# Kernel optimization log

Hardware: AMD Instinct MI355X
Metric: run time of the kernel (lower is better)

## Reference

```python
import jax, jax.numpy as jnp
import numpy as np

# OPT-1.3b-like attention dims
B, S, E, NH, HD = 1, 2048, 2048, 32, 64
Q_BITS, R_BITS, BASE_GS, R_GS = 1, 3, 16, 16


def quotrem_fake_quantize(x, q_bits=Q_BITS, r_bits=R_BITS, base_gs=BASE_GS, r_gs=R_GS):
    r_max = 2 ** (r_bits - 1) - 1
    r_min = -r_max - 1
    eps = 1e-8
    shape = x.shape
    H = shape[-1]
    xg = x.reshape(shape[:-1] + (H // base_gs, base_gs))  # [..., G_base, base_gs]
    max_abs = jnp.maximum(jnp.max(jnp.abs(xg), axis=-1, keepdims=True), eps)
    if q_bits == 1:
        log2_max = jnp.log2(max_abs)
        base_floor = jnp.exp2(jnp.floor(log2_max))
        base_ceil = jnp.exp2(jnp.ceil(log2_max))
        base = jnp.where(jnp.abs(max_abs - base_floor) <= jnp.abs(base_ceil - max_abs),
                         base_floor, base_ceil)
        base = jnp.clip(base, 1.0, 128.0)
        max_pos = jnp.max(xg, axis=-1, keepdims=True)
        min_val = jnp.min(xg, axis=-1, keepdims=True)
        sign_flag = jnp.where(jnp.abs(max_pos) >= jnp.abs(min_val), 1.0, -1.0)
        q = (xg * sign_flag >= base / 2.0).astype(x.dtype)
        q_scaled = q * sign_flag * base
    else:
        q_max = 2 ** (q_bits - 1) - 1
        threshold = max_abs / q_max
        base = jnp.full_like(threshold, 64.0)
        for b in (32.0, 16.0, 8.0, 4.0, 2.0):
            base = jnp.where(threshold <= b, jnp.full_like(threshold, b), base)
        q = jnp.clip(jnp.round(xg / base), -q_max, q_max)
        q_scaled = q * base
    r = (xg - q_scaled).reshape(shape)
    rg = r.reshape(shape[:-1] + (H // r_gs, r_gs))  # [..., G_r, r_gs]
    max_abs_r = jnp.maximum(jnp.max(jnp.abs(rg), axis=-1, keepdims=True), eps)
    scale_r = max_abs_r / r_max
    r_q = jnp.clip(jnp.round(rg / scale_r), r_min, r_max)
    r_dq = (r_q * scale_r).reshape(shape)
    return q_scaled.reshape(shape) + r_dq


def setup_inputs() -> dict:
    key = jax.random.key(0)
    ks = jax.random.split(key, 9)
    w = lambda k: jax.random.normal(k, (E, E), dtype=jnp.float32) * 0.02
    b = lambda k: jax.random.normal(k, (E,), dtype=jnp.float32) * 0.02
    return {
        "hidden_states": jax.random.normal(ks[0], (B, S, E), dtype=jnp.float32),
        "Wq": w(ks[1]), "bq": b(ks[2]),
        "Wk": w(ks[3]), "bk": b(ks[4]),
        "Wv": w(ks[5]), "bv": b(ks[6]),
        "Wo": w(ks[7]), "bo": b(ks[8]),
    }


def reference(hidden_states, Wq, bq, Wk, bk, Wv, bv, Wo, bo):
    scaling = HD ** -0.5
    heads = lambda x: x.reshape(B, S, NH, HD).transpose(0, 2, 1, 3)  # [B,NH,S,HD]
    q = heads((hidden_states @ Wq.T + bq) * scaling)
    k = quotrem_fake_quantize(heads(hidden_states @ Wk.T + bk))
    v = quotrem_fake_quantize(heads(hidden_states @ Wv.T + bv))
    scores = jnp.einsum('bhqd,bhkd->bhqk', q, k)
    idx = jnp.arange(S)
    scores = jnp.where(idx[:, None] >= idx[None, :], scores, -jnp.inf)  # causal
    attn = jax.nn.softmax(scores, axis=-1)
    out = jnp.einsum('bhqk,bhkd->bhqd', attn, v).transpose(0, 2, 1, 3).reshape(B, S, E)
    return out @ Wo.T + bo
```

## Files before the change

### kernel.cpp

```cpp
#include <hip/hip_runtime.h>
#include <math.h>

#define SEQ 2048
#define EMB 2048
#define NHEAD 32
#define HDIM 64

typedef unsigned short u16;
typedef _Float16 half8 __attribute__((ext_vector_type(8)));
typedef _Float16 half4 __attribute__((ext_vector_type(4)));
typedef __attribute__((ext_vector_type(4))) float floatx4;

__device__ __forceinline__ floatx4 mfma_f16(half8 a, half8 b, floatx4 c) {
    return __builtin_amdgcn_mfma_f32_16x16x32_f16(a, b, c, 0, 0, 0);
}
__device__ __forceinline__ void load16(const u16* g, u16* l) {
    __builtin_amdgcn_global_load_lds(
        (const __attribute__((address_space(1))) unsigned int*)g,
        (__attribute__((address_space(3))) unsigned int*)l, 16, 0, 0);
}
__device__ __forceinline__ u16 h2u(_Float16 h) { return *reinterpret_cast<u16*>(&h); }

__global__ __launch_bounds__(256)
void cvt4(const float* __restrict__ X0, u16* __restrict__ Y0,
          const float* __restrict__ X1, u16* __restrict__ Y1,
          const float* __restrict__ X2, u16* __restrict__ Y2,
          const float* __restrict__ X3, u16* __restrict__ Y3)
{
    const float* Xs[4] = {X0, X1, X2, X3};
    u16* Ys[4] = {Y0, Y1, Y2, Y3};
    const float* X = Xs[blockIdx.y];
    u16* Y = Ys[blockIdx.y];
    const int i = (blockIdx.x * 256 + threadIdx.x) * 4;
    float4 v = *reinterpret_cast<const float4*>(X + i);
    half4 hv;
    hv.x = (_Float16)v.x; hv.y = (_Float16)v.y;
    hv.z = (_Float16)v.z; hv.w = (_Float16)v.w;
    *reinterpret_cast<half4*>(Y + i) = hv;
}

__global__ __launch_bounds__(256)
void gemm16(const u16* __restrict__ A,
            const u16* __restrict__ B0, const u16* __restrict__ B1,
            const u16* __restrict__ B2,
            const float* __restrict__ bk, const float* __restrict__ bv,
            const float* __restrict__ bq,
            float* __restrict__ F0, float* __restrict__ F1,
            u16* __restrict__ Qb)
{
    __shared__ __align__(16) u16 As[128 * 64];
    __shared__ __align__(16) u16 Bs[128 * 64];

    const int tid = threadIdx.x;
    const int w = tid >> 6, lane = tid & 63;
    const int quad = lane >> 4, colk = lane & 15;
    const int bn = blockIdx.x, bm = blockIdx.y, z = blockIdx.z;
    const int wm = (w & 1) * 64, wn = (w >> 1) * 64;

    const u16* Bg = (z == 0) ? B0 : (z == 1) ? B1 : B2;

    const int srow = tid >> 3, sphy = tid & 7;
    const int sLog = (sphy - srow) & 7;
    size_t agof[4], bgof[4];
    int ldst[4];
    #pragma unroll
    for (int p = 0; p < 4; ++p) {
        const int row = srow + 32 * p;
        agof[p] = (size_t)(bm * 128 + row) * EMB + sLog * 8;
        bgof[p] = (size_t)(bn * 128 + row) * EMB + sLog * 8;
        ldst[p] = (tid + 256 * p) * 8;
    }

    const int aoct0 = ((quad + colk) & 7) * 8;
    const int aoct1 = ((quad + 4 + colk) & 7) * 8;

    floatx4 acc[4][4];
    #pragma unroll
    for (int i = 0; i < 4; ++i)
        #pragma unroll
        for (int j = 0; j < 4; ++j) acc[i][j] = (floatx4){0.f, 0.f, 0.f, 0.f};

    for (int kt = 0; kt < 2048; kt += 64) {
        __syncthreads();
        #pragma unroll
        for (int p = 0; p < 4; ++p) {
            load16(A  + agof[p] + kt, As + ldst[p]);
            load16(Bg + bgof[p] + kt, Bs + ldst[p]);
        }
        __syncthreads();

        half8 a0[4], a1[4], b0[4], b1[4];
        #pragma unroll
        for (int i = 0; i < 4; ++i) {
            a0[i] = *reinterpret_cast<const half8*>(&As[(wm + 16*i + colk) * 64 + aoct0]);
            a1[i] = *reinterpret_cast<const half8*>(&As[(wm + 16*i + colk) * 64 + aoct1]);
        }
        #pragma unroll
        for (int j = 0; j < 4; ++j) {
            b0[j] = *reinterpret_cast<const half8*>(&Bs[(wn + 16*j + colk) * 64 + aoct0]);
            b1[j] = *reinterpret_cast<const half8*>(&Bs[(wn + 16*j + colk) * 64 + aoct1]);
        }
        #pragma unroll
        for (int i = 0; i < 4; ++i)
            #pragma unroll
            for (int j = 0; j < 4; ++j) {
                acc[i][j] = mfma_f16(a0[i], b0[j], acc[i][j]);
                acc[i][j] = mfma_f16(a1[i], b1[j], acc[i][j]);
            }
    }

    const float* bias = (z == 0) ? bk : (z == 1) ? bv : bq;
    #pragma unroll
    for (int i = 0; i < 4; ++i) {
        const int row = bm * 128 + wm + 16*i + 4*quad;
        #pragma unroll
        for (int j = 0; j < 4; ++j) {
            const int col = bn * 128 + wn + 16*j + colk;
            const float bv2 = bias[col];
            #pragma unroll
            for (int r = 0; r < 4; ++r) {
                const size_t idx = (size_t)(row + r) * EMB + col;
                if (z == 2)
                    ((_Float16*)Qb)[idx] = (_Float16)((acc[i][j][r] + bv2) * 0.125f);
                else
                    ((z == 0) ? F0 : F1)[idx] = acc[i][j][r] + bv2;
            }
        }
    }
}

__device__ __forceinline__ void quotrem16(float* x)
{
    float maxabs = 1e-8f, maxpos = -INFINITY, minval = INFINITY;
    #pragma unroll
    for (int i = 0; i < 16; ++i) {
        maxabs = fmaxf(maxabs, fabsf(x[i]));
        maxpos = fmaxf(maxpos, x[i]);
        minval = fminf(minval, x[i]);
    }
    const float lg = log2f(maxabs);
    const float bfl = exp2f(floorf(lg));
    const float bcl = exp2f(ceilf(lg));
    float base = (fabsf(maxabs - bfl) <= fabsf(bcl - maxabs)) ? bfl : bcl;
    base = fminf(fmaxf(base, 1.0f), 128.0f);
    const float sgn = (fabsf(maxpos) >= fabsf(minval)) ? 1.0f : -1.0f;
    const float hb = 0.5f * base, sb = sgn * base;

    float qs[16], r[16], maxr = 1e-8f;
    #pragma unroll
    for (int i = 0; i < 16; ++i) {
        qs[i] = (x[i] * sgn >= hb) ? sb : 0.0f;
        r[i]  = x[i] - qs[i];
        maxr  = fmaxf(maxr, fabsf(r[i]));
    }
    const float scale = maxr / 3.0f;
    #pragma unroll
    for (int i = 0; i < 16; ++i) {
        float rq = rintf(r[i] / scale);
        rq = fminf(fmaxf(rq, -4.0f), 3.0f);
        x[i] = qs[i] + rq * scale;
    }
}

__global__ __launch_bounds__(256)
void quant_kv(const float* __restrict__ FK, u16* __restrict__ Kb,
              const float* __restrict__ FV, u16* __restrict__ Vt,
              const float* __restrict__ Wo, u16* __restrict__ Wo16)
{
    __shared__ u16 T[64 * 264];
    const int bid = blockIdx.x, t = threadIdx.x;

    if (bid >= 1280) {
        const int i = ((bid - 1280) * 256 + t) * 4;
        float4 v = *reinterpret_cast<const float4*>(Wo + i);
        half4 hv;
        hv.x = (_Float16)v.x; hv.y = (_Float16)v.y;
        hv.z = (_Float16)v.z; hv.w = (_Float16)v.w;
        *reinterpret_cast<half4*>(Wo16 + i) = hv;
        return;
    }

    if (bid < 1024) {
        const int g = bid * 256 + t;
        const float* p = FK + (size_t)g * 16;
        float x[16];
        #pragma unroll
        for (int i = 0; i < 16; i += 4)
            *reinterpret_cast<float4*>(&x[i]) = *reinterpret_cast<const float4*>(p + i);
        quotrem16(x);
        _Float16* o = (_Float16*)Kb + (size_t)g * 16;
        #pragma unroll
        for (int i = 0; i < 16; ++i) o[i] = (_Float16)x[i];
        return;
    }

    const int l = bid - 1024;
    const int sb = l >> 5, h = l & 31;
    const float* src = FV + (size_t)(sb * 256 + t) * EMB + h * HDIM;

    #pragma unroll
    for (int g4 = 0; g4 < 4; ++g4) {
        float x[16];
        #pragma unroll
        for (int i = 0; i < 16; i += 4)
            *reinterpret_cast<float4*>(&x[i]) =
                *reinterpret_cast<const float4*>(src + g4 * 16 + i);
        quotrem16(x);
        #pragma unroll
        for (int i = 0; i < 16; ++i)
            T[(g4 * 16 + i) * 264 + t] = h2u((_Float16)x[i]);
    }
    __syncthreads();

    const int d = t >> 2, seg = t & 3;
    u16* dst = Vt + (size_t)(h * HDIM + d) * SEQ + sb * 256 + seg * 64;
    #pragma unroll
    for (int jj = 0; jj < 8; ++jj)
        *reinterpret_cast<half8*>(dst + jj * 8) =
            *reinterpret_cast<const half8*>(&T[d * 264 + seg * 64 + jj * 8]);
}

__global__ __launch_bounds__(256)
void flash128(const u16* __restrict__ Qb, const u16* __restrict__ Kb,
              const u16* __restrict__ Vt, u16* __restrict__ Ob)
{
    __shared__ __align__(16) u16 Ks[128 * 64];
    __shared__ __align__(16) u16 Vs[64 * 128];
    __shared__ __align__(16) u16 Ps[64 * 136];

    const int tid = threadIdx.x;
    const int w = tid >> 6, lane = tid & 63;
    const int quad = lane >> 4, colk = lane & 15;
    const int id = blockIdx.x;
    const int h = (id & 7) * 4 + ((id >> 3) & 3);
    const int pairb = id >> 5;

    int krow[4], koff[4], vd[4], voff[4];
    #pragma unroll
    for (int p = 0; p < 4; ++p) {
        const int c = tid + p * 256;
        krow[p] = c >> 3;
        koff[p] = (((c & 7) - krow[p]) & 7) * 8;
        vd[p]   = c >> 4;
        voff[p] = (((c & 15) - vd[p]) & 15) * 8;
    }
    const int ldb0 = w * 512;
    const int kp0 = ((quad + colk) & 7) * 8;
    const int kp1 = ((quad + 4 + colk) & 7) * 8;

    #pragma unroll
    for (int pass = 0; pass < 2; ++pass) {
        const int qt = pass ? (31 - pairb) : pairb;
        const int nw = (qt + 2) >> 1;
        const int qrow_g = qt * 64 + 16 * w + colk;

        __syncthreads();
        #pragma unroll
        for (int p = 0; p < 2; ++p) {
            const int c = tid + p * 256, row = c >> 3, cq = c & 7;
            *reinterpret_cast<half8*>(&Ps[row * 136 + cq * 8]) =
                *reinterpret_cast<const half8*>(&Qb[(size_t)(qt * 64 + row) * EMB + h * HDIM + cq * 8]);
        }
        __syncthreads();
        const half8 qb0 = *reinterpret_cast<const half8*>(&Ps[(16*w + colk) * 136 + quad * 8]);
        const half8 qb1 = *reinterpret_cast<const half8*>(&Ps[(16*w + colk) * 136 + 32 + quad * 8]);

        floatx4 o[4];
        #pragma unroll
        for (int t = 0; t < 4; ++t) o[t] = (floatx4){0.f, 0.f, 0.f, 0.f};
        float lsum = 0.f;

        for (int kw = 0; kw < nw; ++kw) {
            __syncthreads();
            #pragma unroll
            for (int p = 0; p < 4; ++p) {
                load16(Kb + (size_t)(kw * 128 + krow[p]) * EMB + h * HDIM + koff[p],
                       Ks + p * 2048 + ldb0);
                load16(Vt + (size_t)(h * HDIM + vd[p]) * SEQ + kw * 128 + voff[p],
                       Vs + p * 2048 + ldb0);
            }
            __syncthreads();

            floatx4 s[8];
            #pragma unroll
            for (int t = 0; t < 8; ++t) {
                const half8 kb0 = *reinterpret_cast<const half8*>(&Ks[(16*t + colk) * 64 + kp0]);
                const half8 kb1 = *reinterpret_cast<const half8*>(&Ks[(16*t + colk) * 64 + kp1]);
                floatx4 zz = (floatx4){0.f, 0.f, 0.f, 0.f};
                zz = mfma_f16(kb0, qb0, zz);
                s[t] = mfma_f16(kb1, qb1, zz);
            }
            if (kw == nw - 1) {
                #pragma unroll
                for (int t = 0; t < 8; ++t)
                    #pragma unroll
                    for (int r = 0; r < 4; ++r)
                        if (kw * 128 + 16*t + 4*quad + r > qrow_g) s[t][r] = -INFINITY;
            }

            #pragma unroll
            for (int t = 0; t < 8; ++t) {
                half4 pw;
                float pv0 = __expf(s[t][0] - 4.0f), pv1 = __expf(s[t][1] - 4.0f);
                float pv2 = __expf(s[t][2] - 4.0f), pv3 = __expf(s[t][3] - 4.0f);
                lsum += (pv0 + pv1) + (pv2 + pv3);
                pw.x = (_Float16)pv0; pw.y = (_Float16)pv1;
                pw.z = (_Float16)pv2; pw.w = (_Float16)pv3;
                *reinterpret_cast<half4*>(&Ps[(16*w + colk) * 136 + 16*t + 4*quad]) = pw;
            }

            half8 pa[4];
            #pragma unroll
            for (int seg = 0; seg < 4; ++seg)
                pa[seg] = *reinterpret_cast<const half8*>(&Ps[(16*w + colk) * 136 + seg * 32 + quad * 8]);
            #pragma unroll
            for (int t = 0; t < 4; ++t) {
                #pragma unroll
                for (int seg = 0; seg < 4; ++seg) {
                    const int vp = ((4*seg + quad + colk) & 15) * 8;
                    const half8 vb = *reinterpret_cast<const half8*>(&Vs[(16*t + colk) * 128 + vp]);
                    o[t] = mfma_f16(pa[seg], vb, o[t]);
                }
            }
        }

        lsum += __shfl_xor(lsum, 16, 64);
        lsum += __shfl_xor(lsum, 32, 64);

        float invr[4];
        #pragma unroll
        for (int r = 0; r < 4; ++r) invr[r] = 1.0f / __shfl(lsum, 4*quad + r, 64);
        #pragma unroll
        for (int t = 0; t < 4; ++t)
            #pragma unroll
            for (int r = 0; r < 4; ++r) {
                const int row = qt * 64 + 16*w + 4*quad + r;
                ((_Float16*)Ob)[(size_t)row * EMB + h * HDIM + 16*t + colk] =
                    (_Float16)(o[t][r] * invr[r]);
            }
    }
}

extern "C" void kernel_launch(void* const* d_in, const int* in_sizes, int n_in,
                              void* d_out, int out_size, void* d_ws, size_t ws_size,
                              hipStream_t stream)
{
    const float* hidden = (const float*)d_in[0];
    const float* Wq = (const float*)d_in[1];
    const float* bq = (const float*)d_in[2];
    const float* Wk = (const float*)d_in[3];
    const float* bk = (const float*)d_in[4];
    const float* Wv = (const float*)d_in[5];
    const float* bv = (const float*)d_in[6];
    const float* Wo = (const float*)d_in[7];
    const float* bo = (const float*)d_in[8];
    float* out = (float*)d_out;

    char* ws = (char*)d_ws;
    const size_t MB = 1024 * 1024;
    u16*   H16  = (u16*)(ws);
    u16*   Wk16 = (u16*)(ws + 8 * MB);
    u16*   Wv16 = (u16*)(ws + 16 * MB);
    float* FK   = (float*)(ws + 24 * MB);
    float* FV   = (float*)(ws + 40 * MB);
    u16*   Qbuf = (u16*)(ws + 56 * MB);
    u16*   Kbuf = (u16*)(ws + 8 * MB);
    u16*   Vtb  = (u16*)(ws + 16 * MB);
    u16*   Wo16 = (u16*)(ws);
    u16*   Obuf = (u16*)(ws + 24 * MB);
    u16*   Wq16 = (u16*)d_out;

    const dim3 cb(256);
    float* nilf = nullptr; u16* nil16 = nullptr;

    hipLaunchKernelGGL(cvt4, dim3(4096, 4), cb, 0, stream,
                       hidden, H16, Wk, Wk16, Wv, Wv16, Wq, Wq16);
    hipLaunchKernelGGL(gemm16, dim3(16, 16, 3), cb, 0, stream,
                       H16, Wk16, Wv16, Wq16, bk, bv, bq, FK, FV, Qbuf);
    hipLaunchKernelGGL(quant_kv, dim3(1280 + 4096), cb, 0, stream,
                       FK, Kbuf, FV, Vtb, Wo, Wo16);
    hipLaunchKernelGGL(flash128, dim3(512), cb, 0, stream,
                       Qbuf, Kbuf, Vtb, Obuf);
    hipLaunchKernelGGL(gemm16, dim3(16, 16, 1), cb, 0, stream,
                       Obuf, Wo16, nil16, nil16, bo, nilf, nilf,
                       out, nilf, nil16);
}
```

Before: 300.3 us.

## Replace QKV projection GEMM with 256x256-tile double-buffered 8-wave pipelined kernel

Adds a new gemm256 kernel for the fused K/V/Q projection. It uses 256x256 output tiles, 512 threads and double-buffered LDS staged through global_load_lds with a swizzled layout. Each k-step is split into four phases that interleave async loads of the next tiles with MFMA work, using explicit waitcnt, barriers and setprio. The goal is more data reuse per tile and hiding global-load latency behind matrix math. The trade-off is a smaller grid (192 blocks) and heavy LDS use per block, which limits occupancy and may leave CUs idle.

Result: no change. 298.3 us (-0.7%).

```diff
diff --git a/kernel.cpp b/kernel.cpp
--- a/kernel.cpp
+++ b/kernel.cpp
@@ -37,6 +37,135 @@
     hv.x = (_Float16)v.x; hv.y = (_Float16)v.y;
     hv.z = (_Float16)v.z; hv.w = (_Float16)v.w;
     *reinterpret_cast<half4*>(Y + i) = hv;
+}
+
+__global__ __launch_bounds__(512, 2)
+void gemm256(const u16* __restrict__ A,
+             const u16* __restrict__ B0, const u16* __restrict__ B1,
+             const u16* __restrict__ B2,
+             const float* __restrict__ bk, const float* __restrict__ bv,
+             const float* __restrict__ bq,
+             float* __restrict__ F0, float* __restrict__ F1,
+             u16* __restrict__ Qb)
+{
+    __shared__ __align__(16) u16 As[2][256 * 64];
+    __shared__ __align__(16) u16 Bs[2][256 * 64];
+
+    const int tid = threadIdx.x;
+    const int w = tid >> 6, lane = tid & 63;
+    const int wm = w >> 2, wn = w & 3;
+    const int quad = lane >> 4, colk = lane & 15;
+    const int lrow = lane >> 3, lphy = lane & 7;
+    const int lsLog = (lphy - lrow) & 7;
+    const int bn = blockIdx.x, bm = blockIdx.y, z = blockIdx.z;
+
+    const u16* Bg  = (z == 0) ? B0 : (z == 1) ? B1 : B2;
+    const u16* Ag  = A  + (size_t)(bm * 256 + lrow) * EMB + lsLog * 8;
+    const u16* Bgp = Bg + (size_t)(bn * 256 + lrow) * EMB + lsLog * 8;
+
+    const int kp0 = ((quad + colk) & 7) * 8;
+    const int kp1 = ((quad + 4 + colk) & 7) * 8;
+    int arow[8], brow[4];
+    #pragma unroll
+    for (int i = 0; i < 8; ++i) arow[i] = (wm * 128 + 16 * i + colk) * 64;
+    #pragma unroll
+    for (int j = 0; j < 4; ++j) brow[j] = (wn * 64 + 16 * j + colk) * 64;
+
+    floatx4 acc[8][4];
+    #pragma unroll
+    for (int i = 0; i < 8; ++i)
+        #pragma unroll
+        for (int j = 0; j < 4; ++j) acc[i][j] = (floatx4){0.f, 0.f, 0.f, 0.f};
+
+#define STAGE_A(MQ, BUF, KT) {                                                \
+    _Pragma("unroll") for (int p_ = 0; p_ < 2; ++p_) {                        \
+        const int r0_ = 128 * p_ + (MQ) * 64 + w * 8;                         \
+        load16(Ag + (size_t)r0_ * EMB + (KT), &As[BUF][r0_ * 64 + lane * 8]); \
+    } }
+#define STAGE_B(NQ, BUF, KT) {                                                \
+    _Pragma("unroll") for (int p_ = 0; p_ < 2; ++p_) {                        \
+        const int b_ = w + 8 * p_;                                            \
+        const int r0_ = 64 * (b_ >> 2) + (NQ) * 32 + (b_ & 3) * 8;            \
+        load16(Bgp + (size_t)r0_ * EMB + (KT), &Bs[BUF][r0_ * 64 + lane * 8]);\
+    } }
+
+#define PHASE(MQ, NQ, BUF, STAGE, GUARD) {                                    \
+    half8 af[4][2], bf[2][2];                                                 \
+    _Pragma("unroll") for (int ii = 0; ii < 4; ++ii) {                        \
+        const u16* ap_ = &As[BUF][arow[4 * (MQ) + ii]];                       \
+        af[ii][0] = *reinterpret_cast<const half8*>(ap_ + kp0);               \
+        af[ii][1] = *reinterpret_cast<const half8*>(ap_ + kp1);               \
+    }                                                                         \
+    _Pragma("unroll") for (int jj = 0; jj < 2; ++jj) {                        \
+        const u16* bp_ = &Bs[BUF][brow[2 * (NQ) + jj]];                       \
+        bf[jj][0] = *reinterpret_cast<const half8*>(bp_ + kp0);               \
+        bf[jj][1] = *reinterpret_cast<const half8*>(bp_ + kp1);               \
+    }                                                                         \
+    STAGE                                                                     \
+    __builtin_amdgcn_s_barrier();                                             \
+    asm volatile("s_waitcnt lgkmcnt(0)" ::: "memory");                        \
+    __builtin_amdgcn_s_setprio(1);                                            \
+    _Pragma("unroll") for (int ii = 0; ii < 4; ++ii)                          \
+        _Pragma("unroll") for (int jj = 0; jj < 2; ++jj) {                    \
+            acc[4*(MQ)+ii][2*(NQ)+jj] =                                       \
+                mfma_f16(af[ii][0], bf[jj][0], acc[4*(MQ)+ii][2*(NQ)+jj]);    \
+            acc[4*(MQ)+ii][2*(NQ)+jj] =                                       \
+                mfma_f16(af[ii][1], bf[jj][1], acc[4*(MQ)+ii][2*(NQ)+jj]);    \
+        }                                                                     \
+    __builtin_amdgcn_s_setprio(0);                                            \
+    if (GUARD) asm volatile("s_waitcnt vmcnt(4)" ::: "memory");               \
+    __builtin_amdgcn_s_barrier();                                             \
+    __builtin_amdgcn_sched_barrier(0);                                        \
+}
+
+    STAGE_B(0, 0, 0)
+    STAGE_A(0, 0, 0)
+    STAGE_A(1, 0, 0)
+    STAGE_B(1, 0, 0)
+    STAGE_B(0, 1, 64)
+    STAGE_A(0, 1, 64)
+    asm volatile("s_waitcnt vmcnt(4)" ::: "memory");
+    __builtin_amdgcn_s_barrier();
+    __builtin_amdgcn_sched_barrier(0);
+
+    #pragma unroll 1
+    for (int it = 0; it < 16; ++it) {
+        const int k1 = ((2 * it + 1) & 31) * 64;
+        const int k2 = ((2 * it + 2) & 31) * 64;
+        const int k3 = ((2 * it + 3) & 31) * 64;
+        PHASE(0, 0, 0, STAGE_A(1, 1, k1), 0)
+        PHASE(1, 0, 0, STAGE_B(1, 1, k1), 0)
+        PHASE(0, 1, 0, STAGE_B(0, 0, k2), 0)
+        PHASE(1, 1, 0, STAGE_A(0, 0, k2), 1)
+        PHASE(0, 0, 1, STAGE_A(1, 0, k2), 0)
+        PHASE(1, 0, 1, STAGE_B(1, 0, k2), 0)
+        PHASE(0, 1, 1, STAGE_B(0, 1, k3), 0)
+        PHASE(1, 1, 1, STAGE_A(0, 1, k3), 1)
+    }
+    asm volatile("s_waitcnt vmcnt(0)" ::: "memory");
+
+#undef STAGE_A
+#undef STAGE_B
+#undef PHASE
+
+    const float* bias = (z == 0) ? bk : (z == 1) ? bv : bq;
+    #pragma unroll
+    for (int i = 0; i < 8; ++i) {
+        const int row = bm * 256 + wm * 128 + 16 * i + 4 * quad;
+        #pragma unroll
+        for (int j = 0; j < 4; ++j) {
+            const int col = bn * 256 + wn * 64 + 16 * j + colk;
+            const float bb = bias[col];
+            #pragma unroll
+            for (int r = 0; r < 4; ++r) {
+                const size_t idx = (size_t)(row + r) * EMB + col;
+                if (z == 2)
+                    ((_Float16*)Qb)[idx] = (_Float16)((acc[i][j][r] + bb) * 0.125f);
+                else
+                    ((z == 0) ? F0 : F1)[idx] = acc[i][j][r] + bb;
+            }
+        }
+    }
 }
 
 __global__ __launch_bounds__(256)
@@ -375,7 +504,7 @@
 
     hipLaunchKernelGGL(cvt4, dim3(4096, 4), cb, 0, stream,
                        hidden, H16, Wk, Wk16, Wv, Wv16, Wq, Wq16);
-    hipLaunchKernelGGL(gemm16, dim3(16, 16, 3), cb, 0, stream,
+    hipLaunchKernelGGL(gemm256, dim3(8, 8, 3), dim3(512), 0, stream,
                        H16, Wk16, Wv16, Wq16, bk, bv, bq, FK, FV, Qbuf);
     hipLaunchKernelGGL(quant_kv, dim3(1280 + 4096), cb, 0, stream,
                        FK, Kbuf, FV, Vtb, Wo, Wo16);
```
